# Performance work log

Hardware: AMD Instinct MI355X
Metric: run time of the kernel (lower is better)

The kernel has to match this reference:

```python
import math
import jax, jax.numpy as jnp
import numpy as np

H = 64  # lstm_hidden_size
T = 9   # seq_len


def _lstm_layer(pre, w_hh):
    """pre: [N, T, 4H] = x @ W_ih^T + b_ih + b_hh; w_hh: [4H, H].
    Returns full hidden sequence [N, T, H]. Gate order (PyTorch): i, f, g, o."""
    N = pre.shape[0]
    pre_t = jnp.transpose(pre, (1, 0, 2))  # [T, N, 4H]
    h0 = jnp.zeros((N, H), dtype=pre.dtype)
    c0 = jnp.zeros((N, H), dtype=pre.dtype)

    def step(carry, xt):
        h, c = carry
        g = xt + h @ w_hh.T  # [N, 4H]
        i = jax.nn.sigmoid(g[:, 0 * H:1 * H])
        f = jax.nn.sigmoid(g[:, 1 * H:2 * H])
        gg = jnp.tanh(g[:, 2 * H:3 * H])
        o = jax.nn.sigmoid(g[:, 3 * H:4 * H])
        c = f * c + i * gg
        h = o * jnp.tanh(c)
        return (h, c), h

    _, hs = jax.lax.scan(step, (h0, c0), pre_t)  # hs: [T, N, H]
    return jnp.transpose(hs, (1, 0, 2))  # [N, T, H]


def _forward(xy, w_ih0, w_hh0, b0, w_ih1, w_hh1, b1,
             fus_w, fus_b, res_w1, res_b1, res_w2, res_b2,
             head_w1, head_b1, head_w2, head_b2):
    x = xy[:, 0:1]
    y = xy[:, 1:2]
    pi = math.pi
    # seq: [N, 9, 1]
    seq = jnp.stack([x, y, x ** 2, y ** 2, x * y,
                     jnp.sin(pi * x), jnp.cos(pi * x),
                     jnp.sin(pi * y), jnp.cos(pi * y)], axis=1)
    # layer 0: input size 1
    pre0 = jnp.einsum('ntd,gd->ntg', seq, w_ih0) + b0  # [N, T, 4H]
    h_seq0 = _lstm_layer(pre0, w_hh0)                   # [N, T, H]
    # layer 1: input size H
    pre1 = jnp.einsum('nth,gh->ntg', h_seq0, w_ih1) + b1
    h_seq1 = _lstm_layer(pre1, w_hh1)
    feat = h_seq1[:, -1, :]                             # [N, H]

    fused = jnp.concatenate([feat, xy], axis=1)         # [N, H+2]
    z = jnp.tanh(fused @ fus_w.T + fus_b)               # [N, 64]
    for k in range(res_w1.shape[0]):
        t = jnp.tanh(z @ res_w1[k].T + res_b1[k])
        z = z + jnp.tanh(t @ res_w2[k].T + res_b2[k])
    h = jnp.tanh(z @ head_w1.T + head_b1)
    return h @ head_w2.T + head_b2                      # [N, 5]


def setup_inputs() -> dict:
    key = jax.random.key(0)
    ks = jax.random.split(key, 20)
    N = 262144
    D = 64  # fc_hidden_dim
    xy = jax.random.uniform(ks[0], (N, 2), dtype=jnp.float32)

    def w(k, shape, scale=0.1):
        return (jax.random.normal(k, shape, dtype=jnp.float32) * scale)

    inp = {
        'xy': xy,
        'w_ih0': w(ks[1], (4 * H, 1)),
        'w_hh0': w(ks[2], (4 * H, H)),
        'b0': jnp.zeros((4 * H,), jnp.float32),
        'w_ih1': w(ks[3], (4 * H, H)),
        'w_hh1': w(ks[4], (4 * H, H)),
        'b1': jnp.zeros((4 * H,), jnp.float32),
        'fus_w': w(ks[5], (D, H + 2)),
        'fus_b': jnp.zeros((D,), jnp.float32),
        'res_w1': w(ks[6], (3, D, D)),
        'res_b1': jnp.zeros((3, D), jnp.float32),
        'res_w2': w(ks[7], (3, D, D)),
        'res_b2': jnp.zeros((3, D), jnp.float32),
        'head_w1': w(ks[8], (D, D)),
        'head_b1': jnp.zeros((D,), jnp.float32),
        'head_w2': w(ks[9], (5, D)),
        'head_b2': jnp.zeros((5,), jnp.float32),
    }
    return inp


def reference(xy, w_ih0, w_hh0, b0, w_ih1, w_hh1, b1,
              fus_w, fus_b, res_w1, res_b1, res_w2, res_b2,
              head_w1, head_b1, head_w2, head_b2):
    return _forward(xy, w_ih0, w_hh0, b0, w_ih1, w_hh1, b1,
                    fus_w, fus_b, res_w1, res_b1, res_w2, res_b2,
                    head_w1, head_b1, head_w2, head_b2)
```

## Files before the change

### kernel.cpp

```cpp
#include <hip/hip_runtime.h>
#include <math.h>

#define PI_F 3.14159265358979323846f
#define WAVES 12
#define TPB (WAVES*64)
#define TPB2 512

typedef _Float16 half_t;
typedef __attribute__((ext_vector_type(8))) _Float16 f16x8;
typedef __attribute__((ext_vector_type(4))) float f32x4;

union F16x8U { f16x8 v; unsigned int u[4]; half_t h[8]; };

__device__ __forceinline__ float frcp(float x)  { return __builtin_amdgcn_rcpf(x); }
__device__ __forceinline__ float ftanh(float x) { return 1.0f - 2.0f * frcp(1.0f + __expf(2.0f * x)); }

__device__ __forceinline__ float2 lstm_gate(float ai, float af, float ag, float ao, float cold) {
    float ui = __expf(-ai);
    float uf = __expf(-af);
    float ug = __expf(-2.0f * ag);
    float uo = __expf(-ao);
    float ig = (1.0f - ug) * frcp((1.0f + ui) * (1.0f + ug));
    float ff = frcp(1.0f + uf);
    float cv = fmaf(ff, cold, ig);
    float uc = __expf(-2.0f * cv);
    float hh = (1.0f - uc) * frcp((1.0f + uo) * (1.0f + uc));
    return make_float2(cv, hh);
}

#define MFMA16(a,b,c) __builtin_amdgcn_mfma_f32_16x16x32_f16((a),(b),(c),0,0,0)

#define AUG_B   98304
#define B1_B    99328
#define EPI_H   50176
#define BIAS_B  172032
#define HOUT_H  88064
#define EF_FUS  0
#define EF_R1   6144
#define EF_R2   18432
#define EF_HW1  30720
#define EF_HW2  34816

__global__ void pack_weights(const float* __restrict__ w_ih0, const float* __restrict__ w_hh0, const float* __restrict__ b0,
                             const float* __restrict__ w_ih1, const float* __restrict__ w_hh1, const float* __restrict__ b1,
                             const float* __restrict__ fus_w, const float* __restrict__ fus_b,
                             const float* __restrict__ res_w1, const float* __restrict__ res_b1,
                             const float* __restrict__ res_w2, const float* __restrict__ res_b2,
                             const float* __restrict__ head_w1, const float* __restrict__ head_b1,
                             const float* __restrict__ head_w2, const float* __restrict__ head_b2,
                             half_t* __restrict__ hws)
{
    int id = blockIdx.x * blockDim.x + threadIdx.x;

    if (id < 6144) {
        int ln = id & 63, rest = id >> 6;
        int kb = rest & 1, cb = (rest >> 1) & 15, mat = rest >> 5;
        const float* W = (mat == 0) ? w_hh0 : ((mat == 1) ? w_ih1 : w_hh1);
        const float* src = W + (cb * 16 + (ln & 15)) * 64 + kb * 32 + (ln >> 4) * 8;
        F16x8U t;
        #pragma unroll
        for (int i = 0; i < 8; ++i) t.h[i] = (half_t)src[i];
        *(f16x8*)&hws[id * 8] = t.v;
        return;
    }
    id -= 6144;
    if (id < 256) {
        F16x8U t; t.u[0] = 0;
        t.h[0] = (half_t)w_ih0[id];
        t.h[1] = (half_t)b0[id];
        ((unsigned int*)((char*)hws + AUG_B))[id] = t.u[0];
        return;
    }
    id -= 256;
    if (id < 256) {
        ((float*)((char*)hws + B1_B))[id] = b1[id];
        return;
    }
    id -= 256;
    if (id < 768) {
        int ln = id & 63, rest = id >> 6;
        int kb = rest % 3, cb = rest / 3;
        int col = cb * 16 + (ln & 15), q = ln >> 4;
        F16x8U t; t.u[0] = t.u[1] = t.u[2] = t.u[3] = 0;
        if (kb < 2) {
            #pragma unroll
            for (int i = 0; i < 8; ++i) t.h[i] = (half_t)fus_w[col * 66 + kb * 32 + q * 8 + i];
        } else if (q == 0) {
            t.h[0] = (half_t)fus_w[col * 66 + 64];
            t.h[1] = (half_t)fus_w[col * 66 + 65];
            t.h[2] = (half_t)fus_b[col];
        }
        *(f16x8*)&hws[(EPI_H + EF_FUS + id * 8)] = t.v;
        return;
    }
    id -= 768;
    if (id < 1536) {
        int ln = id & 63, rest = id >> 6;
        int kb = rest & 1, cb = (rest >> 1) & 3, rb = rest >> 3;
        int col = cb * 16 + (ln & 15), q = ln >> 4;
        F16x8U t;
        #pragma unroll
        for (int i = 0; i < 8; ++i) t.h[i] = (half_t)res_w1[rb * 4096 + col * 64 + kb * 32 + q * 8 + i];
        *(f16x8*)&hws[(EPI_H + EF_R1 + id * 8)] = t.v;
        return;
    }
    id -= 1536;
    if (id < 1536) {
        int ln = id & 63, rest = id >> 6;
        int kb = rest & 1, cb = (rest >> 1) & 3, rb = rest >> 3;
        int col = cb * 16 + (ln & 15), q = ln >> 4;
        F16x8U t;
        #pragma unroll
        for (int i = 0; i < 8; ++i) t.h[i] = (half_t)res_w2[rb * 4096 + col * 64 + kb * 32 + q * 8 + i];
        *(f16x8*)&hws[(EPI_H + EF_R2 + id * 8)] = t.v;
        return;
    }
    id -= 1536;
    if (id < 512) {
        int ln = id & 63, rest = id >> 6;
        int kb = rest & 1, cb = rest >> 1;
        int col = cb * 16 + (ln & 15), q = ln >> 4;
        F16x8U t;
        #pragma unroll
        for (int i = 0; i < 8; ++i) t.h[i] = (half_t)head_w1[col * 64 + kb * 32 + q * 8 + i];
        *(f16x8*)&hws[(EPI_H + EF_HW1 + id * 8)] = t.v;
        return;
    }
    id -= 512;
    if (id < 128) {
        int ln = id & 63, kb = id >> 6;
        int col = ln & 15, q = ln >> 4;
        F16x8U t; t.u[0] = t.u[1] = t.u[2] = t.u[3] = 0;
        if (col < 5) {
            #pragma unroll
            for (int i = 0; i < 8; ++i) t.h[i] = (half_t)head_w2[col * 64 + kb * 32 + q * 8 + i];
        }
        *(f16x8*)&hws[(EPI_H + EF_HW2 + id * 8)] = t.v;
        return;
    }
    id -= 128;
    if (id < 517) {
        float v;
        if      (id < 64)  v = fus_b[id];
        else if (id < 256) v = res_b1[id - 64];
        else if (id < 448) v = res_b2[id - 256];
        else if (id < 512) v = head_b1[id - 448];
        else               v = head_b2[id - 512];
        ((float*)((char*)hws + BIAS_B))[id] = v;
        return;
    }
}

__global__ __launch_bounds__(TPB, 3)
void lstm_core(const float* __restrict__ xy, const half_t* __restrict__ hws, int N)
{
    __shared__ __align__(16) half_t wlds[3][16][2][64][8];
    __shared__ __align__(16) half_t hfrag[WAVES][2][2][64][8];
    __shared__ unsigned int aug_lds[256];
    __shared__ float b1_lds[256];

    const int lane = threadIdx.x & 63;
    const int wid  = threadIdx.x >> 6;
    const int cc   = lane & 15;
    const int qq   = lane >> 4;

    #pragma unroll
    for (int it = 0; it < 8; ++it) {
        int idx = threadIdx.x + it * TPB;
        *(f16x8*)&((half_t*)wlds)[idx * 8] = *(const f16x8*)&hws[idx * 8];
    }
    if (threadIdx.x < 256) {
        aug_lds[threadIdx.x] = ((const unsigned int*)((const char*)hws + AUG_B))[threadIdx.x];
        b1_lds[threadIdx.x]  = ((const float*)((const char*)hws + B1_B))[threadIdx.x];
    }
    __syncthreads();

    const int tile = blockIdx.x * WAVES + wid;
    const int S = tile * 16;
    if (S >= N) return;

    int si = S + cc; if (si >= N) si = N - 1;
    const float fx = xy[2 * si + 0];
    const float fy = xy[2 * si + 1];
    float feat[9];
    feat[0] = fx; feat[1] = fy; feat[2] = fx * fx; feat[3] = fy * fy; feat[4] = fx * fy;
    feat[5] = sinf(PI_F * fx); feat[6] = cosf(PI_F * fx);
    feat[7] = sinf(PI_F * fy); feat[8] = cosf(PI_F * fy);

    {
        F16x8U Z; Z.u[0] = Z.u[1] = Z.u[2] = Z.u[3] = 0;
        *(f16x8*)&hfrag[wid][0][0][lane][0] = Z.v;
        *(f16x8*)&hfrag[wid][0][1][lane][0] = Z.v;
        *(f16x8*)&hfrag[wid][1][0][lane][0] = Z.v;
        *(f16x8*)&hfrag[wid][1][1][lane][0] = Z.v;
    }
    float c0s[4][4], c1s[4][4];
    #pragma unroll
    for (int a = 0; a < 4; ++a)
        #pragma unroll
        for (int b = 0; b < 4; ++b) { c0s[a][b] = 0.0f; c1s[a][b] = 0.0f; }

    asm volatile("" ::: "memory");

    #pragma unroll 1
    for (int t = 0; t < 9; ++t) {
        float ftv;
        switch (t) {
            case 0: ftv = feat[0]; break;  case 1: ftv = feat[1]; break;
            case 2: ftv = feat[2]; break;  case 3: ftv = feat[3]; break;
            case 4: ftv = feat[4]; break;  case 5: ftv = feat[5]; break;
            case 6: ftv = feat[6]; break;  case 7: ftv = feat[7]; break;
            default: ftv = feat[8]; break;
        }
        F16x8U AG; AG.u[0] = AG.u[1] = AG.u[2] = AG.u[3] = 0;
        if (qq == 0) { AG.h[0] = (half_t)ftv; AG.h[1] = (half_t)1.0f; }

        f16x8 a00 = *(const f16x8*)&hfrag[wid][0][0][lane][0];
        f16x8 a01 = *(const f16x8*)&hfrag[wid][0][1][lane][0];
        #pragma unroll
        for (int jj = 0; jj < 4; ++jj) {
            f32x4 acc[4];
            #pragma unroll
            for (int g = 0; g < 4; ++g) {
                const int cb = jj + 4 * g;
                F16x8U BA; BA.u[0] = (qq == 0) ? aug_lds[cb * 16 + cc] : 0u;
                BA.u[1] = 0; BA.u[2] = 0; BA.u[3] = 0;
                f32x4 a = {0.f, 0.f, 0.f, 0.f};
                a = MFMA16(AG.v, BA.v, a);
                f16x8 bf0 = *(const f16x8*)&wlds[0][cb][0][lane][0];
                f16x8 bf1 = *(const f16x8*)&wlds[0][cb][1][lane][0];
                a = MFMA16(a00, bf0, a);
                a = MFMA16(a01, bf1, a);
                acc[g] = a;
            }
            const int kb = jj >> 1;
            half_t* hp = &hfrag[wid][0][kb][0][0];
            const int lb = (4 * qq + 16 * ((2 * jj + (cc >> 3)) & 3)) * 8 + (cc & 7);
            #pragma unroll
            for (int r = 0; r < 4; ++r) {
                float2 ch = lstm_gate(acc[0][r], acc[1][r], acc[2][r], acc[3][r], c0s[jj][r]);
                c0s[jj][r] = ch.x;
                hp[lb + 8 * r] = (half_t)ch.y;
            }
        }
        asm volatile("" ::: "memory");

        f16x8 a10 = *(const f16x8*)&hfrag[wid][0][0][lane][0];
        f16x8 a11 = *(const f16x8*)&hfrag[wid][0][1][lane][0];
        f16x8 a12 = *(const f16x8*)&hfrag[wid][1][0][lane][0];
        f16x8 a13 = *(const f16x8*)&hfrag[wid][1][1][lane][0];
        #pragma unroll
        for (int jj = 0; jj < 4; ++jj) {
            f32x4 acc[4];
            #pragma unroll
            for (int g = 0; g < 4; ++g) {
                const int cb = jj + 4 * g;
                const float bv = b1_lds[cb * 16 + cc];
                f32x4 a = {bv, bv, bv, bv};
                f16x8 bi0 = *(const f16x8*)&wlds[1][cb][0][lane][0];
                f16x8 bi1 = *(const f16x8*)&wlds[1][cb][1][lane][0];
                f16x8 bh0 = *(const f16x8*)&wlds[2][cb][0][lane][0];
                f16x8 bh1 = *(const f16x8*)&wlds[2][cb][1][lane][0];
                a = MFMA16(a10, bi0, a);
                a = MFMA16(a11, bi1, a);
                a = MFMA16(a12, bh0, a);
                a = MFMA16(a13, bh1, a);
                acc[g] = a;
            }
            const int kb = jj >> 1;
            half_t* hp = &hfrag[wid][1][kb][0][0];
            const int lb = (4 * qq + 16 * ((2 * jj + (cc >> 3)) & 3)) * 8 + (cc & 7);
            #pragma unroll
            for (int r = 0; r < 4; ++r) {
                float2 ch = lstm_gate(acc[0][r], acc[1][r], acc[2][r], acc[3][r], c1s[jj][r]);
                c1s[jj][r] = ch.x;
                hp[lb + 8 * r] = (half_t)ch.y;
            }
        }
        asm volatile("" ::: "memory");
    }

    half_t* hout = (half_t*)hws + HOUT_H + (size_t)tile * 1024;
    *(f16x8*)&hout[0   + lane * 8] = *(const f16x8*)&hfrag[wid][1][0][lane][0];
    *(f16x8*)&hout[512 + lane * 8] = *(const f16x8*)&hfrag[wid][1][1][lane][0];
}

__global__ __launch_bounds__(TPB2, 1)
void epi_mlp(const float* __restrict__ xy, const half_t* __restrict__ hws,
             float* __restrict__ out, int ntiles, int N)
{
    __shared__ __align__(16) half_t ef[35840];
    __shared__ float biasl[517];
    __shared__ __align__(16) half_t hbuf[8][2][2][64][8];

    for (int idx = threadIdx.x; idx < 4480; idx += TPB2)
        *(f16x8*)&ef[idx * 8] = *(const f16x8*)&hws[(EPI_H + idx * 8)];
    const float* bg = (const float*)((const char*)hws + BIAS_B);
    for (int i = threadIdx.x; i < 517; i += TPB2) biasl[i] = bg[i];
    __syncthreads();

    const half_t* hout = hws + HOUT_H;
    const int lane = threadIdx.x & 63;
    const int wid  = threadIdx.x >> 6;
    const int cc   = lane & 15;
    const int qq   = lane >> 4;
    const int gw = blockIdx.x * 8 + wid;
    const int nw = gridDim.x * 8;

#define WRITE_ACT(BUF, VALS) do {                                              \
        _Pragma("unroll")                                                      \
        for (int cb = 0; cb < 4; ++cb) {                                       \
            half_t* hp = &hbuf[wid][BUF][cb >> 1][0][0];                       \
            const int lb = (4*qq + 16*((2*cb + (cc>>3)) & 3))*8 + (cc & 7);    \
            _Pragma("unroll")                                                  \
            for (int r = 0; r < 4; ++r) hp[lb + 8*r] = (half_t)(VALS)[cb][r];  \
        }                                                                      \
        asm volatile("" ::: "memory");                                         \
    } while (0)

    #pragma unroll 1
    for (int tile = gw; tile < ntiles; tile += nw) {
        const size_t hob = (size_t)tile * 1024;
        f16x8 e0 = *(const f16x8*)&hout[hob + lane * 8];
        f16x8 e1 = *(const f16x8*)&hout[hob + 512 + lane * 8];

        int s = tile * 16 + cc; if (s >= N) s = N - 1;
        const float fx = xy[2 * s], fy = xy[2 * s + 1];
        F16x8U AF; AF.u[0] = AF.u[1] = AF.u[2] = AF.u[3] = 0;
        if (qq == 0) { AF.h[0] = (half_t)fx; AF.h[1] = (half_t)fy; AF.h[2] = (half_t)1.0f; }

        float zz[4][4];
        #pragma unroll
        for (int cb = 0; cb < 4; ++cb) {
            f32x4 a = {0.f, 0.f, 0.f, 0.f};
            a = MFMA16(e0,   *(const f16x8*)&ef[(EF_FUS + ((cb * 3 + 0) * 64 + lane) * 8)], a);
            a = MFMA16(e1,   *(const f16x8*)&ef[(EF_FUS + ((cb * 3 + 1) * 64 + lane) * 8)], a);
            a = MFMA16(AF.v, *(const f16x8*)&ef[(EF_FUS + ((cb * 3 + 2) * 64 + lane) * 8)], a);
            #pragma unroll
            for (int r = 0; r < 4; ++r) zz[cb][r] = ftanh(a[r]);
        }
        WRITE_ACT(0, zz);
        f16x8 za0 = *(const f16x8*)&hbuf[wid][0][0][lane][0];
        f16x8 za1 = *(const f16x8*)&hbuf[wid][0][1][lane][0];

        #pragma unroll 1
        for (int rb = 0; rb < 3; ++rb) {
            float tt[4][4];
            #pragma unroll
            for (int cb = 0; cb < 4; ++cb) {
                const float bv = biasl[64 + rb * 64 + cb * 16 + cc];
                f32x4 a = {bv, bv, bv, bv};
                a = MFMA16(za0, *(const f16x8*)&ef[(EF_R1 + (((rb * 4 + cb) * 2 + 0) * 64 + lane) * 8)], a);
                a = MFMA16(za1, *(const f16x8*)&ef[(EF_R1 + (((rb * 4 + cb) * 2 + 1) * 64 + lane) * 8)], a);
                #pragma unroll
                for (int r = 0; r < 4; ++r) tt[cb][r] = ftanh(a[r]);
            }
            WRITE_ACT(1, tt);
            f16x8 ta0 = *(const f16x8*)&hbuf[wid][1][0][lane][0];
            f16x8 ta1 = *(const f16x8*)&hbuf[wid][1][1][lane][0];
            #pragma unroll
            for (int cb = 0; cb < 4; ++cb) {
                const float bv = biasl[256 + rb * 64 + cb * 16 + cc];
                f32x4 a = {bv, bv, bv, bv};
                a = MFMA16(ta0, *(const f16x8*)&ef[(EF_R2 + (((rb * 4 + cb) * 2 + 0) * 64 + lane) * 8)], a);
                a = MFMA16(ta1, *(const f16x8*)&ef[(EF_R2 + (((rb * 4 + cb) * 2 + 1) * 64 + lane) * 8)], a);
                #pragma unroll
                for (int r = 0; r < 4; ++r) zz[cb][r] += ftanh(a[r]);
            }
            WRITE_ACT(0, zz);
            za0 = *(const f16x8*)&hbuf[wid][0][0][lane][0];
            za1 = *(const f16x8*)&hbuf[wid][0][1][lane][0];
        }

        float hh[4][4];
        #pragma unroll
        for (int cb = 0; cb < 4; ++cb) {
            const float bv = biasl[448 + cb * 16 + cc];
            f32x4 a = {bv, bv, bv, bv};
            a = MFMA16(za0, *(const f16x8*)&ef[(EF_HW1 + ((cb * 2 + 0) * 64 + lane) * 8)], a);
            a = MFMA16(za1, *(const f16x8*)&ef[(EF_HW1 + ((cb * 2 + 1) * 64 + lane) * 8)], a);
            #pragma unroll
            for (int r = 0; r < 4; ++r) hh[cb][r] = ftanh(a[r]);
        }
        WRITE_ACT(1, hh);
        f16x8 ha0 = *(const f16x8*)&hbuf[wid][1][0][lane][0];
        f16x8 ha1 = *(const f16x8*)&hbuf[wid][1][1][lane][0];

        {
            const float bv = (cc < 5) ? biasl[512 + cc] : 0.0f;
            f32x4 a = {bv, bv, bv, bv};
            a = MFMA16(ha0, *(const f16x8*)&ef[(EF_HW2 + ((0) * 64 + lane) * 8)], a);
            a = MFMA16(ha1, *(const f16x8*)&ef[(EF_HW2 + ((1) * 64 + lane) * 8)], a);
            if (cc < 5) {
                #pragma unroll
                for (int r = 0; r < 4; ++r) {
                    const int row = tile * 16 + 4 * qq + r;
                    if (row < N) out[row * 5 + cc] = a[r];
                }
            }
        }
    }
#undef WRITE_ACT
}

extern "C" void kernel_launch(void* const* d_in, const int* in_sizes, int n_in,
                              void* d_out, int out_size, void* d_ws, size_t ws_size,
                              hipStream_t stream) {
    const float* xy      = (const float*)d_in[0];
    const float* w_ih0   = (const float*)d_in[1];
    const float* w_hh0   = (const float*)d_in[2];
    const float* b0      = (const float*)d_in[3];
    const float* w_ih1   = (const float*)d_in[4];
    const float* w_hh1   = (const float*)d_in[5];
    const float* b1      = (const float*)d_in[6];
    const float* fus_w   = (const float*)d_in[7];
    const float* fus_b   = (const float*)d_in[8];
    const float* res_w1  = (const float*)d_in[9];
    const float* res_b1  = (const float*)d_in[10];
    const float* res_w2  = (const float*)d_in[11];
    const float* res_b2  = (const float*)d_in[12];
    const float* head_w1 = (const float*)d_in[13];
    const float* head_b1 = (const float*)d_in[14];
    const float* head_w2 = (const float*)d_in[15];
    const float* head_b2 = (const float*)d_in[16];

    const int N = in_sizes[0] / 2;
    const int ntiles = (N + 15) / 16;
    half_t* hws = (half_t*)d_ws;

    pack_weights<<<dim3(46), dim3(256), 0, stream>>>(
        w_ih0, w_hh0, b0, w_ih1, w_hh1, b1,
        fus_w, fus_b, res_w1, res_b1, res_w2, res_b2,
        head_w1, head_b1, head_w2, head_b2, hws);

    const int grid1 = (ntiles + WAVES - 1) / WAVES;
    lstm_core<<<dim3(grid1), dim3(TPB), 0, stream>>>(xy, hws, N);

    epi_mlp<<<dim3(256), dim3(TPB2), 0, stream>>>(xy, hws, (float*)d_out, ntiles, N);
}
```

Measured before the change: 529.9 us.

## Fold exp2 gate scaling into packed LSTM weights and use 15 waves per block

Pre-multiplies the LSTM weights and biases by -log2(e), or -2·log2(e) for the g gate, at packing time. The gate nonlinearities can then call the hardware exp2 directly, with no negate or scale multiply per gate element. It also raises the block size from 12 to 15 waves and lowers min-blocks from 3 to 2, which rebalances occupancy against register budget. Scaling before the fp16 conversion changes rounding slightly, and the new block shape may alter register pressure or LDS-limited occupancy.

```diff
diff --git a/kernel.cpp b/kernel.cpp
--- a/kernel.cpp
+++ b/kernel.cpp
@@ -2,9 +2,12 @@
 #include <math.h>
 
 #define PI_F 3.14159265358979323846f
-#define WAVES 12
+#define WAVES 15
 #define TPB (WAVES*64)
 #define TPB2 512
+
+#define GS_IFO (-1.4426950408889634f)
+#define GS_G   (-2.8853900817779268f)
 
 typedef _Float16 half_t;
 typedef __attribute__((ext_vector_type(8))) _Float16 f16x8;
@@ -13,17 +16,18 @@
 union F16x8U { f16x8 v; unsigned int u[4]; half_t h[8]; };
 
 __device__ __forceinline__ float frcp(float x)  { return __builtin_amdgcn_rcpf(x); }
+__device__ __forceinline__ float fexp2(float x) { return __builtin_amdgcn_exp2f(x); }
 __device__ __forceinline__ float ftanh(float x) { return 1.0f - 2.0f * frcp(1.0f + __expf(2.0f * x)); }
 
 __device__ __forceinline__ float2 lstm_gate(float ai, float af, float ag, float ao, float cold) {
-    float ui = __expf(-ai);
-    float uf = __expf(-af);
-    float ug = __expf(-2.0f * ag);
-    float uo = __expf(-ao);
+    float ui = fexp2(ai);
+    float uf = fexp2(af);
+    float ug = fexp2(ag);
+    float uo = fexp2(ao);
     float ig = (1.0f - ug) * frcp((1.0f + ui) * (1.0f + ug));
     float ff = frcp(1.0f + uf);
     float cv = fmaf(ff, cold, ig);
-    float uc = __expf(-2.0f * cv);
+    float uc = fexp2(GS_G * cv);
     float hh = (1.0f - uc) * frcp((1.0f + uo) * (1.0f + uc));
     return make_float2(cv, hh);
 }
@@ -56,24 +60,30 @@
         int ln = id & 63, rest = id >> 6;
         int kb = rest & 1, cb = (rest >> 1) & 15, mat = rest >> 5;
         const float* W = (mat == 0) ? w_hh0 : ((mat == 1) ? w_ih1 : w_hh1);
+        const int gate = cb >> 2;
+        const float sc = (gate == 2) ? GS_G : GS_IFO;
         const float* src = W + (cb * 16 + (ln & 15)) * 64 + kb * 32 + (ln >> 4) * 8;
         F16x8U t;
         #pragma unroll
-        for (int i = 0; i < 8; ++i) t.h[i] = (half_t)src[i];
+        for (int i = 0; i < 8; ++i) t.h[i] = (half_t)(sc * src[i]);
         *(f16x8*)&hws[id * 8] = t.v;
         return;
     }
     id -= 6144;
     if (id < 256) {
+        const int gate = id >> 6;
+        const float sc = (gate == 2) ? GS_G : GS_IFO;
         F16x8U t; t.u[0] = 0;
-        t.h[0] = (half_t)w_ih0[id];
-        t.h[1] = (half_t)b0[id];
+        t.h[0] = (half_t)(sc * w_ih0[id]);
+        t.h[1] = (half_t)(sc * b0[id]);
         ((unsigned int*)((char*)hws + AUG_B))[id] = t.u[0];
         return;
     }
     id -= 256;
     if (id < 256) {
-        ((float*)((char*)hws + B1_B))[id] = b1[id];
+        const int gate = id >> 6;
+        const float sc = (gate == 2) ? GS_G : GS_IFO;
+        ((float*)((char*)hws + B1_B))[id] = sc * b1[id];
         return;
     }
     id -= 256;
@@ -151,7 +161,7 @@
     }
 }
 
-__global__ __launch_bounds__(TPB, 3)
+__global__ __launch_bounds__(TPB, 2)
 void lstm_core(const float* __restrict__ xy, const half_t* __restrict__ hws, int N)
 {
     __shared__ __align__(16) half_t wlds[3][16][2][64][8];
@@ -164,11 +174,8 @@
     const int cc   = lane & 15;
     const int qq   = lane >> 4;
 
-    #pragma unroll
-    for (int it = 0; it < 8; ++it) {
-        int idx = threadIdx.x + it * TPB;
+    for (int idx = threadIdx.x; idx < 6144; idx += TPB)
         *(f16x8*)&((half_t*)wlds)[idx * 8] = *(const f16x8*)&hws[idx * 8];
-    }
     if (threadIdx.x < 256) {
         aug_lds[threadIdx.x] = ((const unsigned int*)((const char*)hws + AUG_B))[threadIdx.x];
         b1_lds[threadIdx.x]  = ((const float*)((const char*)hws + B1_B))[threadIdx.x];
```

New measurement: 514.0 us. 1.03x faster.
